# Optimization experiments

Hardware: AMD Instinct MI355X
Metric: run time of the kernel (lower is better)

The kernel has to match this reference:

```python
import jax, jax.numpy as jnp
import numpy as np

B = 8192
IN_CH = 2048
N_SUB = 8
NETWORK_COUNTS = [150, 148, 132, 136, 76, 122, 236]  # 2 * per-hemi counts
OUT_DIM = sum(NETWORK_COUNTS)  # 1000


def setup_inputs() -> dict:
    key = jax.random.key(0)
    k1, k2, k3, k4 = jax.random.split(key, 4)
    scale = 1.0 / (IN_CH ** 0.5)
    x = jax.random.normal(k1, (B, IN_CH), dtype=jnp.float32)
    subject_ids = jax.random.randint(k2, (B,), 0, N_SUB, dtype=jnp.int64)
    # Concatenation of the 7 per-network SubjectLayers weights along the output
    # dim is mathematically identical to running each head and concatenating.
    W = jax.random.normal(k3, (N_SUB, IN_CH, OUT_DIM), dtype=jnp.float32) * scale
    b = jax.random.normal(k4, (N_SUB, OUT_DIM), dtype=jnp.float32) * scale
    return {"x": x, "subject_ids": subject_ids, "W": W, "b": b}


def reference(x, subject_ids, W, b):
    # out[b, o] = sum_d x[b, d] * W[subject_ids[b], d, o] + bias[subject_ids[b], o]
    # Compute scores against all subjects then select, avoiding materializing
    # the (B, IN_CH, OUT_DIM) gathered weight tensor.
    full = jnp.einsum('bd,sdo->bso', x, W)  # (B, N_SUB, OUT_DIM)
    sel = jnp.take_along_axis(full, subject_ids[:, None, None], axis=1)[:, 0, :]
    return sel + b[subject_ids]
```

## Files before the change

### kernel.cpp

```cpp
#include <hip/hip_runtime.h>
#include <hip/hip_bf16.h>
#include <cstdint>
#include <cstddef>

#define NROWS 8192
#define KDIM  2048
#define ODIM  1000
#define NSUB  8
#define OPAD  1024

#define BM 160
#define BN 256
#define BK 64
#define MT_MAX 8
#define ASLOT (BM * BK)
#define SLOT  ((BM + BN) * BK)

typedef __attribute__((ext_vector_type(4))) float f32x4;
typedef __attribute__((ext_vector_type(8))) short short8v;
typedef __attribute__((ext_vector_type(4))) unsigned short u16x4;
typedef __attribute__((ext_vector_type(4))) int int4v;

__device__ __forceinline__ unsigned short f2bf(float f){
  unsigned u = __builtin_bit_cast(unsigned, f);
  unsigned r = (u + 0x7FFFu + ((u >> 16) & 1u)) >> 16;
  return (unsigned short)r;
}

__device__ __forceinline__ void gload16(const void* g, void* l){
  __builtin_amdgcn_global_load_lds(
      (const __attribute__((address_space(1))) void*)g,
      (__attribute__((address_space(3))) void*)l, 16, 0, 0);
}

__global__ __launch_bounds__(256) void perm_cvt(const int* __restrict__ sid,
                                                int* __restrict__ counts,
                                                int* __restrict__ offsets,
                                                int* __restrict__ perm,
                                                const float* __restrict__ x,
                                                unsigned short* __restrict__ xb){
  int b = blockIdx.x;
  int t = threadIdx.x;

  if (b >= 8){
    size_t base = (size_t)(b - 8) * 8192 + (size_t)t * 8;
    #pragma unroll
    for (int c = 0; c < 4; c++){
      size_t f = base + (size_t)c * 2048;
      f32x4 v0 = *(const f32x4*)(x + f);
      f32x4 v1 = *(const f32x4*)(x + f + 4);
      short8v o;
      o[0] = (short)f2bf(v0[0]); o[1] = (short)f2bf(v0[1]);
      o[2] = (short)f2bf(v0[2]); o[3] = (short)f2bf(v0[3]);
      o[4] = (short)f2bf(v1[0]); o[5] = (short)f2bf(v1[1]);
      o[6] = (short)f2bf(v1[2]); o[7] = (short)f2bf(v1[3]);
      *(short8v*)(xb + f) = o;
    }
    return;
  }

  int s = b;
  __shared__ int shs[NROWS];
  __shared__ int red_lt[4], red_eq[4], wsum[4];
  __shared__ int sh_base;

  int lane = t & 63, wv = t >> 6;
  int c_lt = 0, c_eq = 0;
  const int4v* sv = (const int4v*)sid;
  #pragma unroll
  for (int i = 0; i < NROWS / 4 / 256; i++){
    int idx = i * 256 + t;
    int4v v = sv[idx];
    *(int4v*)&shs[idx * 4] = v;
    #pragma unroll
    for (int e = 0; e < 4; e++){ c_lt += (v[e] < s); c_eq += (v[e] == s); }
  }
  #pragma unroll
  for (int d = 32; d >= 1; d >>= 1){
    c_lt += __shfl_xor(c_lt, d);
    c_eq += __shfl_xor(c_eq, d);
  }
  if (lane == 0){ red_lt[wv] = c_lt; red_eq[wv] = c_eq; }
  __syncthreads();
  if (t == 0){
    int lt = red_lt[0] + red_lt[1] + red_lt[2] + red_lt[3];
    int eq = red_eq[0] + red_eq[1] + red_eq[2] + red_eq[3];
    offsets[s] = lt;
    counts[s]  = eq;
    sh_base = lt;
  }
  __syncthreads();
  int base = sh_base;

  for (int c0 = 0; c0 < NROWS; c0 += 256){
    int v = shs[c0 + t];
    bool eq = (v == s);
    unsigned long long m = __ballot(eq);
    int rk = __popcll(m & ((1ull << lane) - 1ull));
    int wc = __popcll(m);
    if (lane == 0) wsum[wv] = wc;
    __syncthreads();
    int woff = 0;
    #pragma unroll
    for (int w = 0; w < 4; w++) if (w < wv) woff += wsum[w];
    int tot = wsum[0] + wsum[1] + wsum[2] + wsum[3];
    if (eq) perm[base + woff + rk] = c0 + t;
    base += tot;
    __syncthreads();
  }
}

__global__ __launch_bounds__(256) void transpose_w(const float* __restrict__ W,
                                                   unsigned short* __restrict__ Wt){
  __shared__ float tile[64][65];
  int b = blockIdx.x;
  int t = threadIdx.x;
  int s  = b >> 9;
  int kt = (b >> 4) & 31;
  int ot = b & 15;
  int k0 = kt * 64, o0 = ot * 64;

  int kr  = t >> 4;
  int ol4 = (t & 15) * 4;
  bool lval = (o0 + ol4) < ODIM;

  const float* src = W + ((size_t)s * KDIM + k0) * ODIM + o0;
  #pragma unroll
  for (int it = 0; it < 4; it++){
    int k = kr + it * 16;
    f32x4 v = lval ? *(const f32x4*)(src + (size_t)k * ODIM + ol4)
                   : f32x4{0.f, 0.f, 0.f, 0.f};
    tile[k][ol4 + 0] = v[0]; tile[k][ol4 + 1] = v[1];
    tile[k][ol4 + 2] = v[2]; tile[k][ol4 + 3] = v[3];
  }
  __syncthreads();

  int j8   = (t & 7) * 8;
  int orow = t >> 3;
  unsigned short* dst = Wt + ((size_t)(s * OPAD + o0)) * KDIM + k0;
  #pragma unroll
  for (int it = 0; it < 2; it++){
    int o = orow + it * 32;
    bool oval = (o0 + o) < ODIM;
    short8v w;
    #pragma unroll
    for (int j = 0; j < 8; j++)
      w[j] = oval ? (short)f2bf(tile[j8 + j][o]) : (short)0;
    *(short8v*)(dst + (size_t)o * KDIM + j8) = w;
  }
}

__global__ __launch_bounds__(512, 1) void gemm_bf16(
    const unsigned short* __restrict__ xb,
    const unsigned short* __restrict__ Wt,
    const int* __restrict__ counts,
    const int* __restrict__ offsets,
    const int* __restrict__ perm,
    const float* __restrict__ bias,
    float* __restrict__ out)
{
  int b  = blockIdx.x;
  int s  = b & 7;
  int r  = b >> 3;
  int nt = r & 3;
  int mt = r >> 2;
  int cnt = counts[s];
  int loc0 = mt * BM;
  if (loc0 >= cnt) return;
  int row0 = offsets[s] + loc0;
  int cnt_loc = cnt - loc0;

  __shared__ unsigned short L[3 * SLOT];
  __shared__ int permL[BM];

  int t = threadIdx.x;
  int lane = t & 63;
  int wave = t >> 6;

  int wm = (wave >> 2) * 80;
  int wn = (wave & 3) << 6;
  int frow = lane & 15, fk = lane >> 4;
  int axor = frow & 7;

  int srck = (((lane & 7) ^ ((lane >> 3) & 7)) << 3);

  int prow[5];
  if (wave < 4){
    #pragma unroll
    for (int i = 0; i < 5; i++){
      int row = ((wave * 5 + i) << 3) + (lane >> 3);
      int pidx = row0 + row; if (pidx > NROWS - 1) pidx = NROWS - 1;
      prow[i] = perm[pidx];
    }
  }
  {
    int pr = t;
    if (pr >= 320) pr -= 320;
    if (pr >= 160) pr -= 160;
    int pidx = row0 + pr; if (pidx > NROWS - 1) pidx = NROWS - 1;
    int pl = perm[pidx];
    asm volatile("s_waitcnt vmcnt(0)" ::: "memory");
    __builtin_amdgcn_sched_barrier(0);
    permL[pr] = pl;
  }

  size_t gA[5]; unsigned loA[5];
  size_t gB[6]; unsigned loB[6];
  if (wave < 4){
    #pragma unroll
    for (int i = 0; i < 5; i++){
      int ca = wave * 5 + i;
      gA[i]  = (size_t)prow[i] * KDIM + srck;
      loA[i] = (unsigned)((ca << 9) + (lane << 3));
    }
    #pragma unroll
    for (int j = 0; j < 2; j++){
      int cb  = wave * 2 + j;
      int row = (cb << 3) + (lane >> 3);
      gB[j]  = ((size_t)(s * OPAD + nt * BN + row)) * KDIM + srck;
      loB[j] = (unsigned)(ASLOT + (cb << 9) + (lane << 3));
    }
  } else {
    #pragma unroll
    for (int j = 0; j < 6; j++){
      int cb  = 8 + (wave - 4) * 6 + j;
      int row = (cb << 3) + (lane >> 3);
      gB[j]  = ((size_t)(s * OPAD + nt * BN + row)) * KDIM + srck;
      loB[j] = (unsigned)(ASLOT + (cb << 9) + (lane << 3));
    }
  }

  f32x4 acc[5][4];
  #pragma unroll
  for (int i = 0; i < 5; i++)
    #pragma unroll
    for (int j = 0; j < 4; j++)
      #pragma unroll
      for (int e = 0; e < 4; e++) acc[i][j][e] = 0.f;

#define STAGE_FULL(sl, koff) do { \
    unsigned short* Ls = &L[(sl) * SLOT]; \
    if (wave < 4){ \
      gload16(xb + gA[0] + (koff), (void*)(Ls + loA[0])); \
      gload16(xb + gA[1] + (koff), (void*)(Ls + loA[1])); \
      gload16(xb + gA[2] + (koff), (void*)(Ls + loA[2])); \
      gload16(xb + gA[3] + (koff), (void*)(Ls + loA[3])); \
      gload16(xb + gA[4] + (koff), (void*)(Ls + loA[4])); \
      gload16(Wt + gB[0] + (koff), (void*)(Ls + loB[0])); \
      gload16(Wt + gB[1] + (koff), (void*)(Ls + loB[1])); \
    } else { \
      gload16(Wt + gB[0] + (koff), (void*)(Ls + loB[0])); \
      gload16(Wt + gB[1] + (koff), (void*)(Ls + loB[1])); \
      gload16(Wt + gB[2] + (koff), (void*)(Ls + loB[2])); \
      gload16(Wt + gB[3] + (koff), (void*)(Ls + loB[3])); \
      gload16(Wt + gB[4] + (koff), (void*)(Ls + loB[4])); \
      gload16(Wt + gB[5] + (koff), (void*)(Ls + loB[5])); \
    } \
  } while (0)

#define STAGE_P0(sl, koff) do { \
    unsigned short* Ls = &L[(sl) * SLOT]; \
    if (wave < 4){ \
      gload16(xb + gA[0] + (koff), (void*)(Ls + loA[0])); \
      gload16(xb + gA[1] + (koff), (void*)(Ls + loA[1])); \
      gload16(xb + gA[2] + (koff), (void*)(Ls + loA[2])); \
      gload16(xb + gA[3] + (koff), (void*)(Ls + loA[3])); \
      gload16(xb + gA[4] + (koff), (void*)(Ls + loA[4])); \
    } else { \
      gload16(Wt + gB[0] + (koff), (void*)(Ls + loB[0])); \
      gload16(Wt + gB[1] + (koff), (void*)(Ls + loB[1])); \
      gload16(Wt + gB[2] + (koff), (void*)(Ls + loB[2])); \
    } \
  } while (0)
#define STAGE_P1(sl, koff) do { \
    unsigned short* Ls = &L[(sl) * SLOT]; \
    if (wave < 4){ \
      gload16(Wt + gB[0] + (koff), (void*)(Ls + loB[0])); \
      gload16(Wt + gB[1] + (koff), (void*)(Ls + loB[1])); \
    } else { \
      gload16(Wt + gB[3] + (koff), (void*)(Ls + loB[3])); \
      gload16(Wt + gB[4] + (koff), (void*)(Ls + loB[4])); \
      gload16(Wt + gB[5] + (koff), (void*)(Ls + loB[5])); \
    } \
  } while (0)

#define VMN() do { \
    if (wave < 4) asm volatile("s_waitcnt vmcnt(7)" ::: "memory"); \
    else          asm volatile("s_waitcnt vmcnt(6)" ::: "memory"); \
    __builtin_amdgcn_sched_barrier(0); \
  } while (0)
#define VM0() do { \
    asm volatile("s_waitcnt vmcnt(0)" ::: "memory"); \
    __builtin_amdgcn_sched_barrier(0); \
  } while (0)

#define AOFF(mi, ks) (((wm + ((mi) << 4) + frow) << 6) + ((((ks) * 4 + fk) ^ axor) << 3))
#define BOFF(ni, ks) (ASLOT + ((wn + ((ni) << 4) + frow) << 6) + ((((ks) * 4 + fk) ^ axor) << 3))
#define MF(mi, ni, av, bv) acc[mi][ni] = __builtin_amdgcn_mfma_f32_16x16x32_bf16(av, bv, acc[mi][ni], 0, 0, 0)

#define PH(sl, ks, STG) do { \
    const unsigned short* Lb = &L[(sl) * SLOT]; \
    short8v a0 = *(const short8v*)&Lb[AOFF(0, ks)]; \
    short8v a1 = *(const short8v*)&Lb[AOFF(1, ks)]; \
    short8v a2 = *(const short8v*)&Lb[AOFF(2, ks)]; \
    short8v a3 = *(const short8v*)&Lb[AOFF(3, ks)]; \
    short8v a4 = *(const short8v*)&Lb[AOFF(4, ks)]; \
    short8v b0 = *(const short8v*)&Lb[BOFF(0, ks)]; \
    short8v b1 = *(const short8v*)&Lb[BOFF(1, ks)]; \
    short8v b2 = *(const short8v*)&Lb[BOFF(2, ks)]; \
    short8v b3 = *(const short8v*)&Lb[BOFF(3, ks)]; \
    STG; \
    asm volatile("s_waitcnt lgkmcnt(0)" ::: "memory"); \
    __builtin_amdgcn_sched_barrier(0); \
    __builtin_amdgcn_s_setprio(1); \
    MF(0, 0, a0, b0); MF(1, 0, a1, b0); MF(2, 0, a2, b0); MF(3, 0, a3, b0); MF(4, 0, a4, b0); \
    MF(0, 1, a0, b1); MF(1, 1, a1, b1); MF(2, 1, a2, b1); MF(3, 1, a3, b1); MF(4, 1, a4, b1); \
    MF(0, 2, a0, b2); MF(1, 2, a1, b2); MF(2, 2, a2, b2); MF(3, 2, a3, b2); MF(4, 2, a4, b2); \
    MF(0, 3, a0, b3); MF(1, 3, a1, b3); MF(2, 3, a2, b3); MF(3, 3, a3, b3); MF(4, 3, a4, b3); \
    __builtin_amdgcn_s_setprio(0); \
  } while (0)

#define TILE(sl, S0, S1, ENDW) do { \
    PH(sl, 0, S0); \
    PH(sl, 1, S1); \
    ENDW; \
    __builtin_amdgcn_s_barrier(); \
  } while (0)

  STAGE_FULL(0, 0);
  STAGE_FULL(1, BK);
  VMN();
  __builtin_amdgcn_s_barrier();

  for (int i = 0; i < 10; ++i){
    int kb = i * 3 * BK;
    TILE(0, STAGE_P0(2, kb + 2 * BK), STAGE_P1(2, kb + 2 * BK), VMN());
    TILE(1, STAGE_P0(0, kb + 3 * BK), STAGE_P1(0, kb + 3 * BK), VMN());
    TILE(2, STAGE_P0(1, kb + 4 * BK), STAGE_P1(1, kb + 4 * BK), VMN());
  }
  TILE(0, , , VM0());
  PH(1, 0, );
  PH(1, 1, );

  float bvn[4]; int ocol[4];
  #pragma unroll
  for (int ni = 0; ni < 4; ni++){
    int o = nt * BN + wn + (ni << 4) + frow;
    ocol[ni] = o;
    bvn[ni] = (o < ODIM) ? bias[s * ODIM + o] : 0.f;
  }
  #pragma unroll
  for (int mi = 0; mi < 5; mi++){
    int rbase = wm + (mi << 4) + (fk << 2);
    #pragma unroll
    for (int jj = 0; jj < 4; jj++){
      int rr = rbase + jj;
      if (rr < cnt_loc){
        int orow = permL[rr];
        #pragma unroll
        for (int ni = 0; ni < 4; ni++){
          if (ocol[ni] < ODIM)
            out[(size_t)orow * ODIM + ocol[ni]] = acc[mi][ni][jj] + bvn[ni];
        }
      }
    }
  }
#undef STAGE_FULL
#undef STAGE_P0
#undef STAGE_P1
#undef VMN
#undef VM0
#undef AOFF
#undef BOFF
#undef MF
#undef PH
#undef TILE
}

__global__ __launch_bounds__(256) void naive_kernel(const float* __restrict__ x,
                                                    const int* __restrict__ sid,
                                                    const float* __restrict__ W,
                                                    const float* __restrict__ bias,
                                                    float* __restrict__ out){
  __shared__ float xr[KDIM];
  int row = blockIdx.x;
  int s = sid[row];
  for (int i = threadIdx.x; i < KDIM; i += 256) xr[i] = x[(size_t)row * KDIM + i];
  __syncthreads();
  int o = blockIdx.y * 256 + threadIdx.x;
  if (o >= ODIM) return;
  const float* w = W + (size_t)s * KDIM * ODIM + o;
  float acc = bias[s * ODIM + o];
  for (int k = 0; k < KDIM; k++) acc = fmaf(xr[k], w[(size_t)k * ODIM], acc);
  out[(size_t)row * ODIM + o] = acc;
}

extern "C" void kernel_launch(void* const* d_in, const int* in_sizes, int n_in,
                              void* d_out, int out_size, void* d_ws, size_t ws_size,
                              hipStream_t stream) {
  const float* x    = (const float*)d_in[0];
  const int*   sid  = (const int*)d_in[1];
  const float* W    = (const float*)d_in[2];
  const float* bias = (const float*)d_in[3];
  float* out = (float*)d_out;

  const size_t XB_BYTES = (size_t)NROWS * KDIM * 2;
  const size_t WT_BYTES = (size_t)NSUB * OPAD * KDIM * 2;
  const size_t need = 64 + (size_t)NROWS * 4 + XB_BYTES + WT_BYTES;

  if (ws_size < need){
    naive_kernel<<<dim3(NROWS, 4), 256, 0, stream>>>(x, sid, W, bias, out);
    return;
  }

  char* w = (char*)d_ws;
  int* counts  = (int*)w;
  int* offsets = counts + 8;
  int* perm    = (int*)(w + 64);
  unsigned short* xb = (unsigned short*)(w + 64 + (size_t)NROWS * 4);
  unsigned short* Wt = xb + (size_t)NROWS * KDIM;

  perm_cvt    <<<8 + 2048, 256, 0, stream>>>(sid, counts, offsets, perm, x, xb);
  transpose_w <<<4096, 256, 0, stream>>>(W, Wt);
  gemm_bf16   <<<NSUB * 4 * MT_MAX, 512, 0, stream>>>(xb, Wt, counts, offsets, perm, bias, out);
}
```

Measured before the change: 87.39 us.

## Load gathered A rows directly into registers, keep only B in LDS

The permuted x rows (A operand) are no longer staged through LDS. Each wave loads its MFMA A fragments straight from global memory into registers with global_load_dwordx4, double-buffered across K tiles (X/Y). Only the W tile goes through a 3-slot LDS ring, which cuts LDS footprint, LDS read traffic and the perm shared array. In exchange it needs more VGPRs, and because waves with the same rows each load them, A is fetched redundantly from global/L2. The wait counting is also reworked around the new mix of register and LDS loads.

```diff
diff --git a/kernel.cpp b/kernel.cpp
--- a/kernel.cpp
+++ b/kernel.cpp
@@ -13,8 +13,7 @@
 #define BN 256
 #define BK 64
 #define MT_MAX 8
-#define ASLOT (BM * BK)
-#define SLOT  ((BM + BN) * BK)
+#define SLOTB (BN * BK)
 
 typedef __attribute__((ext_vector_type(4))) float f32x4;
 typedef __attribute__((ext_vector_type(8))) short short8v;
@@ -170,8 +169,7 @@
   int row0 = offsets[s] + loc0;
   int cnt_loc = cnt - loc0;
 
-  __shared__ unsigned short L[3 * SLOT];
-  __shared__ int permL[BM];
+  __shared__ unsigned short L[3 * SLOTB];
 
   int t = threadIdx.x;
   int lane = t & 63;
@@ -182,52 +180,29 @@
   int frow = lane & 15, fk = lane >> 4;
   int axor = frow & 7;
 
-  int srck = (((lane & 7) ^ ((lane >> 3) & 7)) << 3);
-
-  int prow[5];
-  if (wave < 4){
-    #pragma unroll
-    for (int i = 0; i < 5; i++){
-      int row = ((wave * 5 + i) << 3) + (lane >> 3);
-      int pidx = row0 + row; if (pidx > NROWS - 1) pidx = NROWS - 1;
-      prow[i] = perm[pidx];
+  unsigned voffA[5];
+  {
+    int prowA[5];
+    #pragma unroll
+    for (int mi = 0; mi < 5; mi++){
+      int rrow = wm + mi * 16 + frow;
+      int pidx = row0 + rrow; if (pidx > NROWS - 1) pidx = NROWS - 1;
+      prowA[mi] = perm[pidx];
     }
-  }
-  {
-    int pr = t;
-    if (pr >= 320) pr -= 320;
-    if (pr >= 160) pr -= 160;
-    int pidx = row0 + pr; if (pidx > NROWS - 1) pidx = NROWS - 1;
-    int pl = perm[pidx];
-    asm volatile("s_waitcnt vmcnt(0)" ::: "memory");
-    __builtin_amdgcn_sched_barrier(0);
-    permL[pr] = pl;
-  }
-
-  size_t gA[5]; unsigned loA[5];
-  size_t gB[6]; unsigned loB[6];
-  if (wave < 4){
-    #pragma unroll
-    for (int i = 0; i < 5; i++){
-      int ca = wave * 5 + i;
-      gA[i]  = (size_t)prow[i] * KDIM + srck;
-      loA[i] = (unsigned)((ca << 9) + (lane << 3));
-    }
-    #pragma unroll
-    for (int j = 0; j < 2; j++){
-      int cb  = wave * 2 + j;
-      int row = (cb << 3) + (lane >> 3);
-      gB[j]  = ((size_t)(s * OPAD + nt * BN + row)) * KDIM + srck;
-      loB[j] = (unsigned)(ASLOT + (cb << 9) + (lane << 3));
-    }
-  } else {
-    #pragma unroll
-    for (int j = 0; j < 6; j++){
-      int cb  = 8 + (wave - 4) * 6 + j;
-      int row = (cb << 3) + (lane >> 3);
-      gB[j]  = ((size_t)(s * OPAD + nt * BN + row)) * KDIM + srck;
-      loB[j] = (unsigned)(ASLOT + (cb << 9) + (lane << 3));
-    }
+    #pragma unroll
+    for (int mi = 0; mi < 5; mi++)
+      voffA[mi] = (unsigned)prowA[mi] * (KDIM * 2) + (unsigned)fk * 16;
+  }
+  asm volatile("s_waitcnt vmcnt(0)" ::: "memory");
+  __builtin_amdgcn_sched_barrier(0);
+
+  int srck = (((t & 7) ^ ((t >> 3) & 7)) << 3);
+  size_t gB[4]; unsigned loB[4];
+  #pragma unroll
+  for (int j = 0; j < 4; j++){
+    int row = (t >> 3) + 64 * j;
+    gB[j]  = ((size_t)(s * OPAD + nt * BN + row)) * KDIM + srck;
+    loB[j] = (unsigned)(((j * 512 + t)) * 8);
   }
 
   f32x4 acc[5][4];
@@ -238,55 +213,34 @@
       #pragma unroll
       for (int e = 0; e < 4; e++) acc[i][j][e] = 0.f;
 
-#define STAGE_FULL(sl, koff) do { \
-    unsigned short* Ls = &L[(sl) * SLOT]; \
-    if (wave < 4){ \
-      gload16(xb + gA[0] + (koff), (void*)(Ls + loA[0])); \
-      gload16(xb + gA[1] + (koff), (void*)(Ls + loA[1])); \
-      gload16(xb + gA[2] + (koff), (void*)(Ls + loA[2])); \
-      gload16(xb + gA[3] + (koff), (void*)(Ls + loA[3])); \
-      gload16(xb + gA[4] + (koff), (void*)(Ls + loA[4])); \
-      gload16(Wt + gB[0] + (koff), (void*)(Ls + loB[0])); \
-      gload16(Wt + gB[1] + (koff), (void*)(Ls + loB[1])); \
-    } else { \
-      gload16(Wt + gB[0] + (koff), (void*)(Ls + loB[0])); \
-      gload16(Wt + gB[1] + (koff), (void*)(Ls + loB[1])); \
-      gload16(Wt + gB[2] + (koff), (void*)(Ls + loB[2])); \
-      gload16(Wt + gB[3] + (koff), (void*)(Ls + loB[3])); \
-      gload16(Wt + gB[4] + (koff), (void*)(Ls + loB[4])); \
-      gload16(Wt + gB[5] + (koff), (void*)(Ls + loB[5])); \
-    } \
-  } while (0)
-
-#define STAGE_P0(sl, koff) do { \
-    unsigned short* Ls = &L[(sl) * SLOT]; \
-    if (wave < 4){ \
-      gload16(xb + gA[0] + (koff), (void*)(Ls + loA[0])); \
-      gload16(xb + gA[1] + (koff), (void*)(Ls + loA[1])); \
-      gload16(xb + gA[2] + (koff), (void*)(Ls + loA[2])); \
-      gload16(xb + gA[3] + (koff), (void*)(Ls + loA[3])); \
-      gload16(xb + gA[4] + (koff), (void*)(Ls + loA[4])); \
-    } else { \
-      gload16(Wt + gB[0] + (koff), (void*)(Ls + loB[0])); \
-      gload16(Wt + gB[1] + (koff), (void*)(Ls + loB[1])); \
-      gload16(Wt + gB[2] + (koff), (void*)(Ls + loB[2])); \
-    } \
-  } while (0)
-#define STAGE_P1(sl, koff) do { \
-    unsigned short* Ls = &L[(sl) * SLOT]; \
-    if (wave < 4){ \
-      gload16(Wt + gB[0] + (koff), (void*)(Ls + loB[0])); \
-      gload16(Wt + gB[1] + (koff), (void*)(Ls + loB[1])); \
-    } else { \
-      gload16(Wt + gB[3] + (koff), (void*)(Ls + loB[3])); \
-      gload16(Wt + gB[4] + (koff), (void*)(Ls + loB[4])); \
-      gload16(Wt + gB[5] + (koff), (void*)(Ls + loB[5])); \
-    } \
+  short8v X[5][2], Y[5][2];
+
+#define GLA(dst, voff, IMM) \
+  asm volatile("global_load_dwordx4 %0, %1, %2 offset:" IMM \
+               : "=v"(dst) : "v"(voff), "s"(xb))
+
+#define LDA(P) do { \
+    GLA(P[0][0], voffA[0], "0"); GLA(P[0][1], voffA[0], "64"); \
+    GLA(P[1][0], voffA[1], "0"); GLA(P[1][1], voffA[1], "64"); \
+    GLA(P[2][0], voffA[2], "0"); GLA(P[2][1], voffA[2], "64"); \
+    GLA(P[3][0], voffA[3], "0"); GLA(P[3][1], voffA[3], "64"); \
+    GLA(P[4][0], voffA[4], "0"); GLA(P[4][1], voffA[4], "64"); \
+    _Pragma("unroll") \
+    for (int mi = 0; mi < 5; mi++) voffA[mi] += 128; \
+    __builtin_amdgcn_sched_barrier(0); \
+  } while (0)
+
+#define STAGEB(sl, koff) do { \
+    unsigned short* Ls = &L[(sl) * SLOTB]; \
+    gload16(Wt + gB[0] + (koff), (void*)(Ls + loB[0])); \
+    gload16(Wt + gB[1] + (koff), (void*)(Ls + loB[1])); \
+    gload16(Wt + gB[2] + (koff), (void*)(Ls + loB[2])); \
+    gload16(Wt + gB[3] + (koff), (void*)(Ls + loB[3])); \
+    __builtin_amdgcn_sched_barrier(0); \
   } while (0)
 
 #define VMN() do { \
-    if (wave < 4) asm volatile("s_waitcnt vmcnt(7)" ::: "memory"); \
-    else          asm volatile("s_waitcnt vmcnt(6)" ::: "memory"); \
+    asm volatile("s_waitcnt vmcnt(4)" ::: "memory"); \
     __builtin_amdgcn_sched_barrier(0); \
   } while (0)
 #define VM0() do { \
@@ -294,53 +248,57 @@
     __builtin_amdgcn_sched_barrier(0); \
   } while (0)
 
-#define AOFF(mi, ks) (((wm + ((mi) << 4) + frow) << 6) + ((((ks) * 4 + fk) ^ axor) << 3))
-#define BOFF(ni, ks) (ASLOT + ((wn + ((ni) << 4) + frow) << 6) + ((((ks) * 4 + fk) ^ axor) << 3))
+#define BOFF(ni, ks) (((wn + ((ni) << 4) + frow) << 6) + ((((ks) * 4 + fk) ^ axor) << 3))
 #define MF(mi, ni, av, bv) acc[mi][ni] = __builtin_amdgcn_mfma_f32_16x16x32_bf16(av, bv, acc[mi][ni], 0, 0, 0)
 
-#define PH(sl, ks, STG) do { \
-    const unsigned short* Lb = &L[(sl) * SLOT]; \
-    short8v a0 = *(const short8v*)&Lb[AOFF(0, ks)]; \
-    short8v a1 = *(const short8v*)&Lb[AOFF(1, ks)]; \
-    short8v a2 = *(const short8v*)&Lb[AOFF(2, ks)]; \
-    short8v a3 = *(const short8v*)&Lb[AOFF(3, ks)]; \
-    short8v a4 = *(const short8v*)&Lb[AOFF(4, ks)]; \
-    short8v b0 = *(const short8v*)&Lb[BOFF(0, ks)]; \
-    short8v b1 = *(const short8v*)&Lb[BOFF(1, ks)]; \
-    short8v b2 = *(const short8v*)&Lb[BOFF(2, ks)]; \
-    short8v b3 = *(const short8v*)&Lb[BOFF(3, ks)]; \
+#define MFMA40(P, BF) do { \
+    __builtin_amdgcn_s_setprio(1); \
+    _Pragma("unroll") \
+    for (int ks = 0; ks < 2; ks++) \
+      _Pragma("unroll") \
+      for (int mi = 0; mi < 5; mi++) \
+        _Pragma("unroll") \
+        for (int ni = 0; ni < 4; ni++) \
+          MF(mi, ni, P[mi][ks], BF[ni][ks]); \
+    __builtin_amdgcn_s_setprio(0); \
+  } while (0)
+
+#define TILE(sl, CUR, LDAP, STG, ENDW) do { \
+    const unsigned short* Lb = &L[(sl) * SLOTB]; \
+    short8v bf[4][2]; \
+    _Pragma("unroll") \
+    for (int ks = 0; ks < 2; ks++) \
+      _Pragma("unroll") \
+      for (int ni = 0; ni < 4; ni++) \
+        bf[ni][ks] = *(const short8v*)&Lb[BOFF(ni, ks)]; \
+    __builtin_amdgcn_sched_barrier(0); \
+    LDAP; \
     STG; \
     asm volatile("s_waitcnt lgkmcnt(0)" ::: "memory"); \
     __builtin_amdgcn_sched_barrier(0); \
-    __builtin_amdgcn_s_setprio(1); \
-    MF(0, 0, a0, b0); MF(1, 0, a1, b0); MF(2, 0, a2, b0); MF(3, 0, a3, b0); MF(4, 0, a4, b0); \
-    MF(0, 1, a0, b1); MF(1, 1, a1, b1); MF(2, 1, a2, b1); MF(3, 1, a3, b1); MF(4, 1, a4, b1); \
-    MF(0, 2, a0, b2); MF(1, 2, a1, b2); MF(2, 2, a2, b2); MF(3, 2, a3, b2); MF(4, 2, a4, b2); \
-    MF(0, 3, a0, b3); MF(1, 3, a1, b3); MF(2, 3, a2, b3); MF(3, 3, a3, b3); MF(4, 3, a4, b3); \
-    __builtin_amdgcn_s_setprio(0); \
-  } while (0)
-
-#define TILE(sl, S0, S1, ENDW) do { \
-    PH(sl, 0, S0); \
-    PH(sl, 1, S1); \
+    MFMA40(CUR, bf); \
     ENDW; \
     __builtin_amdgcn_s_barrier(); \
   } while (0)
 
-  STAGE_FULL(0, 0);
-  STAGE_FULL(1, BK);
-  VMN();
+  LDA(X);
+  STAGEB(0, 0);
+  STAGEB(1, BK);
+  asm volatile("s_waitcnt vmcnt(4)" ::: "memory");
+  __builtin_amdgcn_sched_barrier(0);
   __builtin_amdgcn_s_barrier();
 
-  for (int i = 0; i < 10; ++i){
-    int kb = i * 3 * BK;
-    TILE(0, STAGE_P0(2, kb + 2 * BK), STAGE_P1(2, kb + 2 * BK), VMN());
-    TILE(1, STAGE_P0(0, kb + 3 * BK), STAGE_P1(0, kb + 3 * BK), VMN());
-    TILE(2, STAGE_P0(1, kb + 4 * BK), STAGE_P1(1, kb + 4 * BK), VMN());
-  }
-  TILE(0, , , VM0());
-  PH(1, 0, );
-  PH(1, 1, );
+  for (int i = 0; i < 5; ++i){
+    int kb = i * 6 * BK;
+    TILE(0, X, LDA(Y), STAGEB(2, kb + 2 * BK), VMN());
+    TILE(1, Y, LDA(X), STAGEB(0, kb + 3 * BK), VMN());
+    TILE(2, X, LDA(Y), STAGEB(1, kb + 4 * BK), VMN());
+    TILE(0, Y, LDA(X), STAGEB(2, kb + 5 * BK), VMN());
+    TILE(1, X, LDA(Y), STAGEB(0, kb + 6 * BK), VMN());
+    TILE(2, Y, LDA(X), STAGEB(1, kb + 7 * BK), VMN());
+  }
+  TILE(0, X, LDA(Y), , VM0());
+  TILE(1, Y, , , );
 
   float bvn[4]; int ocol[4];
   #pragma unroll
@@ -356,7 +314,7 @@
     for (int jj = 0; jj < 4; jj++){
       int rr = rbase + jj;
       if (rr < cnt_loc){
-        int orow = permL[rr];
+        int orow = perm[row0 + rr];
         #pragma unroll
         for (int ni = 0; ni < 4; ni++){
           if (ocol[ni] < ODIM)
@@ -365,15 +323,14 @@
       }
     }
   }
-#undef STAGE_FULL
-#undef STAGE_P0
-#undef STAGE_P1
+#undef GLA
+#undef LDA
+#undef STAGEB
 #undef VMN
 #undef VM0
-#undef AOFF
 #undef BOFF
 #undef MF
-#undef PH
+#undef MFMA40
 #undef TILE
 }
 
```

Measured after the change: 139.6 us. +59.7%, slower.
